# Kernel tuning notes

Measured on AMD Instinct MI355X. Metric: run time of the kernel, lower is better.

The kernel has to match this reference:

```python
import jax, jax.numpy as jnp
import numpy as np

RATIO = 0.25
RADIUS = 0.2
NSAMPLE = 32


def fps(xyz, S):
    """Farthest point sampling. xyz: [B,N,3] -> indices [B,S] (int32)."""
    B, N, _ = xyz.shape

    def step(carry, _):
        min_d, last_idx = carry  # [B,N], [B]
        centroid = jnp.take_along_axis(xyz, last_idx[:, None, None], axis=1)  # [B,1,3]
        d = jnp.sum((xyz - centroid) ** 2, axis=-1)  # [B,N]
        min_d = jnp.minimum(min_d, d)
        nxt = jnp.argmax(min_d, axis=-1).astype(jnp.int32)
        return (min_d, nxt), last_idx

    init = (jnp.full((B, N), 1e10, xyz.dtype), jnp.zeros((B,), jnp.int32))
    _, idxs = jax.lax.scan(step, init, None, length=S)  # [S,B]
    return idxs.T  # [B,S]


def ball_query(radius, nsample, xyz, new_xyz):
    """xyz: [B,N,3], new_xyz: [B,S,3] -> group idx [B,S,nsample] (int32)."""
    B, S, _ = new_xyz.shape
    N = xyz.shape[1]
    sqd = jnp.sum((new_xyz[:, :, None, :] - xyz[:, None, :, :]) ** 2, axis=-1)  # [B,S,N]
    idx = jnp.broadcast_to(jnp.arange(N, dtype=jnp.int32), (B, S, N))
    idx = jnp.where(sqd > radius * radius, N, idx)
    idx = jnp.sort(idx, axis=-1)[:, :, :nsample]  # first nsample in-ball ids (ascending)
    first = idx[:, :, :1]
    idx = jnp.where(idx == N, first, idx)  # pad empties with first neighbor
    return idx


def reference(xyz, features, W1, b1, W2, b2):
    B, N, _ = xyz.shape
    S = int(N * RATIO)
    fps_idx = fps(xyz, S)  # [B,S]
    new_xyz = jnp.take_along_axis(xyz, fps_idx[:, :, None], axis=1)  # [B,S,3]
    grp_idx = ball_query(RADIUS, NSAMPLE, xyz, new_xyz)  # [B,S,K]
    batch = jnp.arange(B, dtype=jnp.int32)[:, None, None]
    new_points = features[batch, grp_idx]  # [B,S,K,D]
    # shared MLP (1x1 Conv2d equivalents) + ReLU
    h = jax.nn.relu(jnp.einsum('bskd,ed->bske', new_points, W1) + b1)
    h = jax.nn.relu(jnp.einsum('bskd,ed->bske', h, W2) + b2)
    new_points_out = jnp.max(h, axis=2)  # max over group K -> [B,S,D']
    new_points_out = new_points_out.transpose(0, 2, 1)  # [B,D',S]
    new_xyz_out = new_xyz.transpose(0, 2, 1)  # [B,3,S]
    return new_xyz_out, new_points_out


def setup_inputs() -> dict:
    key = jax.random.key(0)
    k1, k2, k3, k4 = jax.random.split(key, 4)
    B, N, D = 16, 4096, 64
    xyz = jax.random.uniform(k1, (B, N, 3), dtype=jnp.float32)
    features = jax.random.normal(k2, (B, N, D), dtype=jnp.float32)
    W1 = jax.random.normal(k3, (64, 64), dtype=jnp.float32) * (1.0 / np.sqrt(64))
    b1 = jnp.zeros((64,), jnp.float32)
    W2 = jax.random.normal(k4, (128, 64), dtype=jnp.float32) * (1.0 / np.sqrt(64))
    b2 = jnp.zeros((128,), jnp.float32)
    return {"xyz": xyz, "features": features, "W1": W1, "b1": b1, "W2": W2, "b2": b2}
```

## Files before the change

### kernel.cpp

```cpp
#include <hip/hip_runtime.h>
#include <hip/hip_bf16.h>

#define BATCH 16
#define NPTS  4096
#define NSAMP 1024
#define KNB   32
#define DFEAT 64

#define THREADS  512
#define FPS_PPT  (NPTS / THREADS)
#define NWV      (THREADS / 64)
#define NWBLK    240
#define NWAVES   (NWBLK * NWV)
#define NTASK    (BATCH * NSAMP)
#define TAG_BASE 0xC0FFEE00u

template <int CTRL, int RMASK>
__device__ __forceinline__ void dpp_round(unsigned long long& key) {
    const int klo = (int)(unsigned)key;
    const int khi = (int)(unsigned)(key >> 32);
    const int tlo = __builtin_amdgcn_update_dpp(klo, klo, CTRL, RMASK, 0xF, false);
    const int thi = __builtin_amdgcn_update_dpp(khi, khi, CTRL, RMASK, 0xF, false);
    const unsigned long long tk =
        ((unsigned long long)(unsigned)thi << 32) | (unsigned)tlo;
    if (tk > key) key = tk;
}

__device__ __forceinline__ void pub_store(unsigned long long* p, unsigned long long v) {
    __hip_atomic_store(p, v, __ATOMIC_RELAXED, __HIP_MEMORY_SCOPE_AGENT);
}
__device__ __forceinline__ unsigned long long pub_load(const unsigned long long* p) {
    return __hip_atomic_load(p, __ATOMIC_RELAXED, __HIP_MEMORY_SCOPE_AGENT);
}

__device__ __forceinline__ void barrier_lds_only() {
    asm volatile("s_waitcnt lgkmcnt(0)" ::: "memory");
    __builtin_amdgcn_s_barrier();
}

__global__ __launch_bounds__(THREADS) void fused_kernel(
    const float* __restrict__ xyz, const float* __restrict__ features,
    const float* __restrict__ W1, const float* __restrict__ b1,
    const float* __restrict__ W2, const float* __restrict__ b2,
    float* __restrict__ out_xyz, float* __restrict__ out_pts,
    unsigned long long* __restrict__ pub) {

    __shared__ alignas(16) unsigned char smem[65536 + 12288 + 128];
    const int bid  = blockIdx.x;
    const int tid  = threadIdx.x;
    const int lane = tid & 63;
    const int wid  = tid >> 6;

    if (bid < BATCH) {
        float4* sc = (float4*)smem;
        float* stX = (float*)(smem + 65536);
        float* stY = stX + NSAMP;
        float* stZ = stY + NSAMP;
        unsigned long long* pw = (unsigned long long*)(smem + 65536 + 12288);

        float px[FPS_PPT], py[FPS_PPT], pz[FPS_PPT], md[FPS_PPT];
        const float* base = xyz + (size_t)bid * NPTS * 3;
#pragma unroll
        for (int j = 0; j < FPS_PPT; j++) {
            const int i = j * THREADS + tid;
            const float x = base[i * 3 + 0];
            const float y = base[i * 3 + 1];
            const float z = base[i * 3 + 2];
            sc[i] = make_float4(x, y, z, 0.0f);
            px[j] = x; py[j] = y; pz[j] = z;
            md[j] = 1e10f;
        }

        float cx = base[0], cy = base[1], cz = base[2];
        unsigned long long* pb = pub + (size_t)bid * NSAMP * 3;
        if (tid == 0) {
            stX[0] = cx; stY[0] = cy; stZ[0] = cz;
            pub_store(&pb[0], ((unsigned long long)__float_as_uint(cx) << 32) | (TAG_BASE + 0));
            pub_store(&pb[1], ((unsigned long long)__float_as_uint(cy) << 32) | (TAG_BASE + 0));
            pub_store(&pb[2], ((unsigned long long)__float_as_uint(cz) << 32) | (TAG_BASE + 0));
        }
        __syncthreads();

        for (int s = 1; s < NSAMP; s++) {
            float best = -1.0f;
            int   bj   = 0;
#pragma unroll
            for (int j = 0; j < FPS_PPT; j++) {
                const float dx = px[j] - cx;
                const float dy = py[j] - cy;
                const float dz = pz[j] - cz;
                const float d = __fadd_rn(__fadd_rn(__fmul_rn(dx, dx), __fmul_rn(dy, dy)),
                                          __fmul_rn(dz, dz));
                const float m = fminf(md[j], d);
                md[j] = m;
                if (m > best) { best = m; bj = j; }
            }
            const int bi = (bj << 9) | tid;
            unsigned long long key =
                ((unsigned long long)__float_as_uint(best) << 32) | (unsigned)(~bi);
            dpp_round<0x111, 0xF>(key);
            dpp_round<0x112, 0xF>(key);
            dpp_round<0x114, 0xF>(key);
            dpp_round<0x118, 0xF>(key);
            dpp_round<0x142, 0xA>(key);
            dpp_round<0x143, 0xC>(key);

            const int par = s & 1;
            if (lane == 63) pw[par * NWV + wid] = key;
            barrier_lds_only();
            const ulong2 p01 = *(const ulong2*)&pw[par * NWV + 0];
            const ulong2 p23 = *(const ulong2*)&pw[par * NWV + 2];
            const ulong2 p45 = *(const ulong2*)&pw[par * NWV + 4];
            const ulong2 p67 = *(const ulong2*)&pw[par * NWV + 6];
            unsigned long long bk = p01.x;
            if (p01.y > bk) bk = p01.y;
            if (p23.x > bk) bk = p23.x;
            if (p23.y > bk) bk = p23.y;
            if (p45.x > bk) bk = p45.x;
            if (p45.y > bk) bk = p45.y;
            if (p67.x > bk) bk = p67.x;
            if (p67.y > bk) bk = p67.y;
            const int bix = (int)(~(unsigned)bk);

            const float4 c = sc[bix];
            cx = c.x; cy = c.y; cz = c.z;
            if (tid == 0) {
                stX[s] = cx; stY[s] = cy; stZ[s] = cz;
                pub_store(&pb[3 * s + 0], ((unsigned long long)__float_as_uint(cx) << 32) | (TAG_BASE + s));
                pub_store(&pb[3 * s + 1], ((unsigned long long)__float_as_uint(cy) << 32) | (TAG_BASE + s));
                pub_store(&pb[3 * s + 2], ((unsigned long long)__float_as_uint(cz) << 32) | (TAG_BASE + s));
            }
        }

        __syncthreads();
        float* ob = out_xyz + (size_t)bid * 3 * NSAMP;
        for (int i = tid; i < NSAMP; i += THREADS) {
            ob[0 * NSAMP + i] = stX[i];
            ob[1 * NSAMP + i] = stY[i];
            ob[2 * NSAMP + i] = stZ[i];
        }
    } else {
        float (*xls)[KNB][DFEAT] = (float (*)[KNB][DFEAT])smem;
        float (*h1s)[DFEAT]      = (float (*)[DFEAT])(smem + 65536);
        int   (*gl)[KNB]         = (int (*)[KNB])(smem + 65536 + 2048);

        float w1r[64], w2ra[64], w2rb[64];
        {
            const float4* W1v = (const float4*)(W1 + (size_t)lane * 64);
            const float4* W2a = (const float4*)(W2 + (size_t)lane * 64);
            const float4* W2b = (const float4*)(W2 + (size_t)(lane + 64) * 64);
#pragma unroll
            for (int i = 0; i < 16; i++) {
                float4 v = W1v[i];
                w1r[4 * i] = v.x; w1r[4 * i + 1] = v.y; w1r[4 * i + 2] = v.z; w1r[4 * i + 3] = v.w;
                v = W2a[i];
                w2ra[4 * i] = v.x; w2ra[4 * i + 1] = v.y; w2ra[4 * i + 2] = v.z; w2ra[4 * i + 3] = v.w;
                v = W2b[i];
                w2rb[4 * i] = v.x; w2rb[4 * i + 1] = v.y; w2rb[4 * i + 2] = v.z; w2rb[4 * i + 3] = v.w;
            }
        }
        const float b1r  = b1[lane];
        const float b2ra = b2[lane];
        const float b2rb = b2[lane + 64];

        const int gwave = (bid - BATCH) * NWV + wid;
        for (int t = gwave; t < NTASK; t += NWAVES) {
            const int sq = t >> 4;
            const int b  = t & 15;

            const unsigned long long* pp = pub + ((size_t)b * NSAMP + sq) * 3;
            const unsigned exp_tag = TAG_BASE + sq;
            float pxf = 0.0f, pyf = 0.0f, pzf = 0.0f;
            if (lane == 0) {
                unsigned long long w0, w1, w2;
                for (;;) {
                    w0 = pub_load(&pp[0]);
                    w1 = pub_load(&pp[1]);
                    w2 = pub_load(&pp[2]);
                    if ((unsigned)w0 == exp_tag && (unsigned)w1 == exp_tag &&
                        (unsigned)w2 == exp_tag) break;
                    __builtin_amdgcn_s_sleep(2);
                }
                pxf = __uint_as_float((unsigned)(w0 >> 32));
                pyf = __uint_as_float((unsigned)(w1 >> 32));
                pzf = __uint_as_float((unsigned)(w2 >> 32));
            }
            const float cx = __shfl(pxf, 0);
            const float cy = __shfl(pyf, 0);
            const float cz = __shfl(pzf, 0);

            const float* base = xyz + (size_t)b * NPTS * 3;
            const float r2 = 0.04f;
            int cnt = 0;
            int firstCand = 0x7fffffff;
            for (int bp = 0; bp < NPTS && cnt < KNB; bp += 64) {
                const int p = bp + lane;
                const float dx = base[p * 3 + 0] - cx;
                const float dy = base[p * 3 + 1] - cy;
                const float dz = base[p * 3 + 2] - cz;
                const float d = __fadd_rn(__fadd_rn(__fmul_rn(dx, dx), __fmul_rn(dy, dy)),
                                          __fmul_rn(dz, dz));
                const bool ok = !(d > r2);
                const unsigned long long m = __ballot(ok);
                const int rank = cnt + (int)__popcll(m & ((1ull << lane) - 1ull));
                if (ok && rank < KNB) gl[wid][rank] = p;
                if (ok && rank == 0) firstCand = p;
                cnt += (int)__popcll(m);
            }
            const int found = cnt < KNB ? cnt : KNB;
            if (found < KNB) {
#pragma unroll
                for (int off = 32; off > 0; off >>= 1) {
                    const int o = __shfl_xor(firstCand, off);
                    firstCand = o < firstCand ? o : firstCand;
                }
                for (int r = found + lane; r < KNB; r += 64) gl[wid][r] = firstCand;
            }
            int gi = 0;
            if (lane < KNB) gi = gl[wid][lane];

            const float* fb = features + (size_t)b * NPTS * DFEAT;
            for (int k = 0; k < KNB; k++) {
                const int idxk = __shfl(gi, k);
                xls[wid][k][lane] = fb[(size_t)idxk * DFEAT + lane];
            }

            float m0 = 0.0f, m1 = 0.0f;
            for (int k = 0; k < KNB; k++) {
                float acc = b1r;
                const float4* xk = (const float4*)xls[wid][k];
#pragma unroll
                for (int i = 0; i < 16; i++) {
                    const float4 v = xk[i];
                    acc = fmaf(v.x, w1r[4 * i], acc);
                    acc = fmaf(v.y, w1r[4 * i + 1], acc);
                    acc = fmaf(v.z, w1r[4 * i + 2], acc);
                    acc = fmaf(v.w, w1r[4 * i + 3], acc);
                }
                h1s[wid][lane] = fmaxf(acc, 0.0f);
                float a0 = b2ra, a1 = b2rb;
                const float4* hv4 = (const float4*)h1s[wid];
#pragma unroll
                for (int i = 0; i < 16; i++) {
                    const float4 v = hv4[i];
                    a0 = fmaf(v.x, w2ra[4 * i], a0);
                    a0 = fmaf(v.y, w2ra[4 * i + 1], a0);
                    a0 = fmaf(v.z, w2ra[4 * i + 2], a0);
                    a0 = fmaf(v.w, w2ra[4 * i + 3], a0);
                    a1 = fmaf(v.x, w2rb[4 * i], a1);
                    a1 = fmaf(v.y, w2rb[4 * i + 1], a1);
                    a1 = fmaf(v.z, w2rb[4 * i + 2], a1);
                    a1 = fmaf(v.w, w2rb[4 * i + 3], a1);
                }
                m0 = fmaxf(m0, fmaxf(a0, 0.0f));
                m1 = fmaxf(m1, fmaxf(a1, 0.0f));
            }

            out_pts[(size_t)b * 128 * NSAMP + (size_t)lane * NSAMP + sq]        = m0;
            out_pts[(size_t)b * 128 * NSAMP + (size_t)(lane + 64) * NSAMP + sq] = m1;
        }
    }
}

extern "C" void kernel_launch(void* const* d_in, const int* in_sizes, int n_in,
                              void* d_out, int out_size, void* d_ws, size_t ws_size,
                              hipStream_t stream) {
    const float* xyz      = (const float*)d_in[0];
    const float* features = (const float*)d_in[1];
    const float* W1       = (const float*)d_in[2];
    const float* b1       = (const float*)d_in[3];
    const float* W2       = (const float*)d_in[4];
    const float* b2       = (const float*)d_in[5];

    float* out_xyz = (float*)d_out;
    float* out_pts = (float*)d_out + (size_t)BATCH * 3 * NSAMP;

    unsigned long long* pub = (unsigned long long*)d_ws;

    fused_kernel<<<BATCH + NWBLK, THREADS, 0, stream>>>(
        xyz, features, W1, b1, W2, b2, out_xyz, out_pts, pub);
}
```

Baseline: 667.7 us.

## Pack FPS distance math into v_pk f32 ops and move xyz output to workers

Rewrites the FPS inner distance loop to use packed two-wide f32 add and multiply instructions, which roughly halves the VALU instruction count on the serial critical path. It replaces the linear max chain over the wave keys with a tree reduction. It also drops the LDS staging of sampled centroids and the final output loop in the FPS blocks; instead the worker waves write out_xyz for each task they consume. This cuts LDS use and the FPS tail, though sq must be defined in the hidden worker code.

```diff
diff --git a/kernel.cpp b/kernel.cpp
--- a/kernel.cpp
+++ b/kernel.cpp
@@ -14,6 +14,19 @@
 #define NWAVES   (NWBLK * NWV)
 #define NTASK    (BATCH * NSAMP)
 #define TAG_BASE 0xC0FFEE00u
+
+typedef float v2f __attribute__((ext_vector_type(2)));
+
+__device__ __forceinline__ v2f pk_add(v2f a, v2f b) {
+    v2f r;
+    asm("v_pk_add_f32 %0, %1, %2" : "=v"(r) : "v"(a), "v"(b));
+    return r;
+}
+__device__ __forceinline__ v2f pk_mul(v2f a, v2f b) {
+    v2f r;
+    asm("v_pk_mul_f32 %0, %1, %2" : "=v"(r) : "v"(a), "v"(b));
+    return r;
+}
 
 template <int CTRL, int RMASK>
 __device__ __forceinline__ void dpp_round(unsigned long long& key) {
@@ -45,7 +58,7 @@
     float* __restrict__ out_xyz, float* __restrict__ out_pts,
     unsigned long long* __restrict__ pub) {
 
-    __shared__ alignas(16) unsigned char smem[65536 + 12288 + 128];
+    __shared__ alignas(16) unsigned char smem[65536 + 4096];
     const int bid  = blockIdx.x;
     const int tid  = threadIdx.x;
     const int lane = tid & 63;
@@ -53,28 +66,27 @@
 
     if (bid < BATCH) {
         float4* sc = (float4*)smem;
-        float* stX = (float*)(smem + 65536);
-        float* stY = stX + NSAMP;
-        float* stZ = stY + NSAMP;
-        unsigned long long* pw = (unsigned long long*)(smem + 65536 + 12288);
-
-        float px[FPS_PPT], py[FPS_PPT], pz[FPS_PPT], md[FPS_PPT];
+        unsigned long long* pw = (unsigned long long*)(smem + 65536);
+
+        v2f Px[4], Py[4], Pz[4], Md[4];
         const float* base = xyz + (size_t)bid * NPTS * 3;
 #pragma unroll
-        for (int j = 0; j < FPS_PPT; j++) {
-            const int i = j * THREADS + tid;
-            const float x = base[i * 3 + 0];
-            const float y = base[i * 3 + 1];
-            const float z = base[i * 3 + 2];
-            sc[i] = make_float4(x, y, z, 0.0f);
-            px[j] = x; py[j] = y; pz[j] = z;
-            md[j] = 1e10f;
+        for (int jj = 0; jj < 4; jj++) {
+#pragma unroll
+            for (int h = 0; h < 2; h++) {
+                const int i = (2 * jj + h) * THREADS + tid;
+                const float x = base[i * 3 + 0];
+                const float y = base[i * 3 + 1];
+                const float z = base[i * 3 + 2];
+                sc[i] = make_float4(x, y, z, 0.0f);
+                Px[jj][h] = x; Py[jj][h] = y; Pz[jj][h] = z;
+                Md[jj][h] = 1e10f;
+            }
         }
 
         float cx = base[0], cy = base[1], cz = base[2];
         unsigned long long* pb = pub + (size_t)bid * NSAMP * 3;
         if (tid == 0) {
-            stX[0] = cx; stY[0] = cy; stZ[0] = cz;
             pub_store(&pb[0], ((unsigned long long)__float_as_uint(cx) << 32) | (TAG_BASE + 0));
             pub_store(&pb[1], ((unsigned long long)__float_as_uint(cy) << 32) | (TAG_BASE + 0));
             pub_store(&pb[2], ((unsigned long long)__float_as_uint(cz) << 32) | (TAG_BASE + 0));
@@ -82,18 +94,26 @@
         __syncthreads();
 
         for (int s = 1; s < NSAMP; s++) {
+            const v2f ncx = {-cx, -cx};
+            const v2f ncy = {-cy, -cy};
+            const v2f ncz = {-cz, -cz};
             float best = -1.0f;
             int   bj   = 0;
 #pragma unroll
-            for (int j = 0; j < FPS_PPT; j++) {
-                const float dx = px[j] - cx;
-                const float dy = py[j] - cy;
-                const float dz = pz[j] - cz;
-                const float d = __fadd_rn(__fadd_rn(__fmul_rn(dx, dx), __fmul_rn(dy, dy)),
-                                          __fmul_rn(dz, dz));
-                const float m = fminf(md[j], d);
-                md[j] = m;
-                if (m > best) { best = m; bj = j; }
+            for (int jj = 0; jj < 4; jj++) {
+                const v2f dx = pk_add(Px[jj], ncx);
+                const v2f dy = pk_add(Py[jj], ncy);
+                const v2f dz = pk_add(Pz[jj], ncz);
+                const v2f xx = pk_mul(dx, dx);
+                const v2f yy = pk_mul(dy, dy);
+                const v2f zz = pk_mul(dz, dz);
+                const v2f d  = pk_add(pk_add(xx, yy), zz);
+                const float m0 = fminf(Md[jj][0], d[0]);
+                const float m1 = fminf(Md[jj][1], d[1]);
+                Md[jj][0] = m0;
+                Md[jj][1] = m1;
+                if (m0 > best) { best = m0; bj = 2 * jj; }
+                if (m1 > best) { best = m1; bj = 2 * jj + 1; }
             }
             const int bi = (bj << 9) | tid;
             unsigned long long key =
@@ -112,32 +132,22 @@
             const ulong2 p23 = *(const ulong2*)&pw[par * NWV + 2];
             const ulong2 p45 = *(const ulong2*)&pw[par * NWV + 4];
             const ulong2 p67 = *(const ulong2*)&pw[par * NWV + 6];
-            unsigned long long bk = p01.x;
-            if (p01.y > bk) bk = p01.y;
-            if (p23.x > bk) bk = p23.x;
-            if (p23.y > bk) bk = p23.y;
-            if (p45.x > bk) bk = p45.x;
-            if (p45.y > bk) bk = p45.y;
-            if (p67.x > bk) bk = p67.x;
-            if (p67.y > bk) bk = p67.y;
+            unsigned long long t0 = p01.x > p01.y ? p01.x : p01.y;
+            unsigned long long t1 = p23.x > p23.y ? p23.x : p23.y;
+            unsigned long long t2 = p45.x > p45.y ? p45.x : p45.y;
+            unsigned long long t3 = p67.x > p67.y ? p67.x : p67.y;
+            t0 = t0 > t1 ? t0 : t1;
+            t2 = t2 > t3 ? t2 : t3;
+            const unsigned long long bk = t0 > t2 ? t0 : t2;
             const int bix = (int)(~(unsigned)bk);
 
             const float4 c = sc[bix];
             cx = c.x; cy = c.y; cz = c.z;
             if (tid == 0) {
-                stX[s] = cx; stY[s] = cy; stZ[s] = cz;
                 pub_store(&pb[3 * s + 0], ((unsigned long long)__float_as_uint(cx) << 32) | (TAG_BASE + s));
                 pub_store(&pb[3 * s + 1], ((unsigned long long)__float_as_uint(cy) << 32) | (TAG_BASE + s));
                 pub_store(&pb[3 * s + 2], ((unsigned long long)__float_as_uint(cz) << 32) | (TAG_BASE + s));
             }
-        }
-
-        __syncthreads();
-        float* ob = out_xyz + (size_t)bid * 3 * NSAMP;
-        for (int i = tid; i < NSAMP; i += THREADS) {
-            ob[0 * NSAMP + i] = stX[i];
-            ob[1 * NSAMP + i] = stY[i];
-            ob[2 * NSAMP + i] = stZ[i];
         }
     } else {
         float (*xls)[KNB][DFEAT] = (float (*)[KNB][DFEAT])smem;
@@ -188,6 +198,13 @@
             const float cx = __shfl(pxf, 0);
             const float cy = __shfl(pyf, 0);
             const float cz = __shfl(pzf, 0);
+
+            if (lane == 0) {
+                float* ob = out_xyz + (size_t)b * 3 * NSAMP;
+                ob[0 * NSAMP + sq] = cx;
+                ob[1 * NSAMP + sq] = cy;
+                ob[2 * NSAMP + sq] = cz;
+            }
 
             const float* base = xyz + (size_t)b * NPTS * 3;
             const float r2 = 0.04f;
```

New measurement: 705.8 us. 1.06x slower.
